# Kernel tuning notes

Measured on AMD Instinct MI355X. Metric: run time of the kernel, lower is better.

The kernel has to match this reference:

```python
import jax, jax.numpy as jnp
import numpy as np

N_HEAD = 16


def setup_inputs() -> dict:
    key = jax.random.key(0)
    k1, k2, k3 = jax.random.split(key, 3)
    B, T, C = 2, 2048, 1024
    x = jax.random.normal(k1, (B, T, C), dtype=jnp.float32)
    Wqkv = jax.random.normal(k2, (C, 3 * C), dtype=jnp.float32) * 0.02
    bqkv = jnp.zeros((3 * C,), dtype=jnp.float32)
    Wproj = jax.random.normal(k3, (C, C), dtype=jnp.float32) * 0.02
    bproj = jnp.zeros((C,), dtype=jnp.float32)
    return {"x": x, "Wqkv": Wqkv, "bqkv": bqkv, "Wproj": Wproj, "bproj": bproj}


def reference(x, Wqkv, bqkv, Wproj, bproj):
    b, t, c = x.shape
    h = N_HEAD
    d = c // h  # head_dim
    # qkv projection, split into q,k,v per head: (b,t,3,h,d)
    qkv = (x @ Wqkv + bqkv).reshape(b, t, 3, h, d)
    q, k, v = qkv[:, :, 0], qkv[:, :, 1], qkv[:, :, 2]  # each (b,t,h,d)
    # Faithful quirk of original: n_state = head_dim // heads, scale = 1/sqrt(n_state)
    scale = jnp.float32(1.0 / np.sqrt(d // h))
    # attn_mode == 'all': dense non-causal attention
    w = jnp.einsum('bqhd,bkhd->bhqk', q, k)  # (b,h,t,t)
    w = jax.nn.softmax(w * scale, axis=-1)
    a = jnp.einsum('bhqk,bkhd->bqhd', w, v).reshape(b, t, c)
    return a @ Wproj + bproj
```

## Files before the change

kernel.cpp:

```cpp
#include <hip/hip_runtime.h>

typedef float floatx4 __attribute__((ext_vector_type(4)));
typedef __bf16 bf16x8 __attribute__((ext_vector_type(8)));
typedef __bf16 bf16x4 __attribute__((ext_vector_type(4)));

#define MFMA16 __builtin_amdgcn_mfma_f32_16x16x32_bf16

typedef const __attribute__((address_space(1))) void* gas_t;
typedef __attribute__((address_space(3))) void* las_t;
#define GLD16(g, l) __builtin_amdgcn_global_load_lds((gas_t)(g), (las_t)(l), 16, 0, 0)

static __device__ __forceinline__ unsigned short f2bf(float f) {
  union { float f; unsigned int u; } v; v.f = f;
  unsigned int r = v.u + 0x7fffu + ((v.u >> 16) & 1u);
  return (unsigned short)(r >> 16);
}

static __device__ __forceinline__ void cast_transpose_tile(
    const float* __restrict__ in, unsigned short* __restrict__ out,
    int R, int C, int bx, int by) {
  const int r0 = by * 64, c0 = bx * 64;
  const int tid = threadIdx.x;
  __shared__ float tl[64][65];
  const int rr = tid >> 4, cc = (tid & 15) * 4;
#pragma unroll
  for (int i = 0; i < 4; ++i) {
    int row = rr + i * 16;
    float4 v = *(const float4*)(in + (size_t)(r0 + row) * C + c0 + cc);
    tl[row][cc] = v.x; tl[row][cc + 1] = v.y;
    tl[row][cc + 2] = v.z; tl[row][cc + 3] = v.w;
  }
  __syncthreads();
  const int cl = tid >> 2, rbase = (tid & 3) * 16;
  unsigned short o[16];
#pragma unroll
  for (int j = 0; j < 16; ++j) o[j] = f2bf(tl[rbase + j][cl]);
  unsigned short* dst = out + (size_t)(c0 + cl) * R + r0 + rbase;
  *(uint4*)dst = *(uint4*)o;
  *(uint4*)(dst + 8) = *(uint4*)(o + 8);
}

__global__ __launch_bounds__(256) void prologue_kernel(
    const float* __restrict__ x, unsigned short* __restrict__ Xb,
    const float* __restrict__ Wqkv, unsigned short* __restrict__ Wqkvt,
    const float* __restrict__ Wproj, unsigned short* __restrict__ Wprojt) {
  const int bid = blockIdx.x;
  if (bid < 4096) {
    int i = bid * 256 + threadIdx.x;
    float4 v = ((const float4*)x)[i];
    ushort4 o;
    o.x = f2bf(v.x); o.y = f2bf(v.y); o.z = f2bf(v.z); o.w = f2bf(v.w);
    ((ushort4*)Xb)[i] = o;
  } else if (bid < 4096 + 768) {
    int b2 = bid - 4096;
    cast_transpose_tile(Wqkv, Wqkvt, 1024, 3072, b2 % 48, b2 / 48);
  } else {
    int b3 = bid - 4096 - 768;
    cast_transpose_tile(Wproj, Wprojt, 1024, 1024, b3 % 16, b3 / 16);
  }
}

__global__ __launch_bounds__(256) void gemm_qkv(
    const unsigned short* __restrict__ A,
    const unsigned short* __restrict__ Bt,
    const float* __restrict__ bias,
    unsigned short* __restrict__ Q,
    unsigned short* __restrict__ Kc,
    unsigned short* __restrict__ Vt) {
  const int K = 1024;
  const int m0 = blockIdx.y * 128, n0 = blockIdx.x * 128;
  const int tid = threadIdx.x, w = tid >> 6, l = tid & 63;
  const int l16 = l & 15, lq = l >> 4;
  const int wm = w >> 1, wn = w & 1;
  const int which = n0 >> 10;

  __shared__ unsigned short As[128 * 64];
  __shared__ unsigned short Bs[128 * 64];

  floatx4 acc[4][4] = {};

  int sA[4], sB[4];
  unsigned ldso[4];
#pragma unroll
  for (int j = 0; j < 4; ++j) {
    int s = j * 256 + tid;
    int row = s >> 3, blk = (s & 7) ^ (row & 7);
    sA[j] = (m0 + row) * K + blk * 8;
    sB[j] = (n0 + row) * K + blk * 8;
    ldso[j] = (unsigned)(j * 256 + w * 64) * 8;
  }

  if (which == 2) {
    for (int k0 = 0; k0 < K; k0 += 64) {
      __syncthreads();
#pragma unroll
      for (int j = 0; j < 4; ++j) {
        GLD16(A + sA[j] + k0, As + ldso[j]);
        GLD16(Bt + sB[j] + k0, Bs + ldso[j]);
      }
      __syncthreads();
#pragma unroll
      for (int kk = 0; kk < 2; ++kk) {
        bf16x8 af[4], bf[4];
#pragma unroll
        for (int mi = 0; mi < 4; ++mi) {
          int row = wm * 64 + mi * 16 + l16;
          int blk = (kk * 4 + lq) ^ (l16 & 7);
          af[mi] = *(const bf16x8*)(As + row * 64 + blk * 8);
        }
#pragma unroll
        for (int ni = 0; ni < 4; ++ni) {
          int row = wn * 64 + ni * 16 + l16;
          int blk = (kk * 4 + lq) ^ (l16 & 7);
          bf[ni] = *(const bf16x8*)(Bs + row * 64 + blk * 8);
        }
#pragma unroll
        for (int ni = 0; ni < 4; ++ni)
#pragma unroll
          for (int mi = 0; mi < 4; ++mi)
            acc[mi][ni] = MFMA16(af[mi], bf[ni], acc[mi][ni], 0, 0, 0);
      }
    }
    float bv[4];
#pragma unroll
    for (int ni = 0; ni < 4; ++ni) bv[ni] = bias[n0 + wn * 64 + ni * 16 + l16];
#pragma unroll
    for (int mi = 0; mi < 4; ++mi) {
#pragma unroll
      for (int ni = 0; ni < 4; ++ni) {
        int col = n0 + wn * 64 + ni * 16 + l16;
        int c1 = col & 1023;
        int h = c1 >> 6, dd = c1 & 63;
        int row0 = m0 + wm * 64 + mi * 16 + lq * 4;
        int bb = row0 >> 11, tt0 = row0 & 2047;
        size_t bh = (size_t)(bb * 16 + h);
        floatx4 vv = acc[mi][ni] + bv[ni];
        *(bf16x4*)(Vt + (bh * 64 + dd) * 2048 + tt0) =
            __builtin_convertvector(vv, bf16x4);
      }
    }
  } else {
    for (int k0 = 0; k0 < K; k0 += 64) {
      __syncthreads();
#pragma unroll
      for (int j = 0; j < 4; ++j) {
        GLD16(A + sA[j] + k0, As + ldso[j]);
        GLD16(Bt + sB[j] + k0, Bs + ldso[j]);
      }
      __syncthreads();
#pragma unroll
      for (int kk = 0; kk < 2; ++kk) {
        bf16x8 af[4], bf[4];
#pragma unroll
        for (int mi = 0; mi < 4; ++mi) {
          int row = wm * 64 + mi * 16 + l16;
          int blk = (kk * 4 + lq) ^ (l16 & 7);
          af[mi] = *(const bf16x8*)(As + row * 64 + blk * 8);
        }
#pragma unroll
        for (int ni = 0; ni < 4; ++ni) {
          int row = wn * 64 + ni * 16 + l16;
          int blk = (kk * 4 + lq) ^ (l16 & 7);
          bf[ni] = *(const bf16x8*)(Bs + row * 64 + blk * 8);
        }
#pragma unroll
        for (int ni = 0; ni < 4; ++ni)
#pragma unroll
          for (int mi = 0; mi < 4; ++mi)
            acc[mi][ni] = MFMA16(bf[ni], af[mi], acc[mi][ni], 0, 0, 0);
      }
    }
    const float sc = (which == 0) ? 0.7213475204444817f : 1.0f;
    unsigned short* dst = (which == 0) ? Q : Kc;
#pragma unroll
    for (int mi = 0; mi < 4; ++mi) {
      int t_g = m0 + wm * 64 + mi * 16 + l16;
      int bb = t_g >> 11, tt = t_g & 2047;
#pragma unroll
      for (int ni = 0; ni < 4; ++ni) {
        int col0 = n0 + wn * 64 + ni * 16 + lq * 4;
        floatx4 bv = *(const floatx4*)(bias + col0);
        floatx4 vv = (acc[mi][ni] + bv) * sc;
        int h = (col0 & 1023) >> 6, dd0 = col0 & 63;
        size_t bh = (size_t)(bb * 16 + h);
        *(bf16x4*)(dst + (bh * 2048 + tt) * 64 + dd0) =
            __builtin_convertvector(vv, bf16x4);
      }
    }
  }
}

__global__ __launch_bounds__(512, 2) void attn_kernel(
    const unsigned short* __restrict__ Q,
    const unsigned short* __restrict__ Kc,
    const unsigned short* __restrict__ Vt,
    unsigned short* __restrict__ AO) {
  const int T = 2048;
  const int bh = blockIdx.y, q0 = blockIdx.x * 256;
  const int tid = threadIdx.x, w = tid >> 6, l = tid & 63;
  const int l16 = l & 15, lq = l >> 4;
  const int kh = w >> 2, wq = w & 3;
  const int h256 = tid & 255;

  __shared__ unsigned short KVs[2][2][2][4096];
  __shared__ unsigned short Ps[8][64 * 64];
  __shared__ float Lx[4][4][64];

  bf16x8 qf[4][2];
  {
    const unsigned short* qb = Q + ((size_t)bh * T + q0 + wq * 64) * 64;
#pragma unroll
    for (int qs = 0; qs < 4; ++qs) {
      const unsigned short* qr = qb + (qs * 16 + l16) * 64;
      qf[qs][0] = *(const bf16x8*)(qr + lq * 8);
      qf[qs][1] = *(const bf16x8*)(qr + 32 + lq * 8);
    }
  }

  float l_lane[4] = {0.f, 0.f, 0.f, 0.f};
  floatx4 o_acc[4][4] = {};

  const unsigned short* kbase = Kc + (size_t)bh * T * 64;
  const unsigned short* vbase = Vt + (size_t)bh * 64 * T;
  int kro[2], vro[2];
  unsigned ldso[2];
#pragma unroll
  for (int j = 0; j < 2; ++j) {
    int s = j * 256 + h256;
    int row = s >> 3, blk = (s & 7) ^ (row & 7);
    kro[j] = row * 64 + blk * 8;
    vro[j] = row * T + blk * 8;
    ldso[j] = (unsigned)(j * 256 + wq * 64) * 8;
  }

  const int swz0 = (0 + lq) ^ (l16 & 7);
  const int swz1 = (4 + lq) ^ (l16 & 7);
  unsigned short* pw = Ps[w];

  {
    int c0 = kh * 16;
#pragma unroll
    for (int j = 0; j < 2; ++j) {
      GLD16(kbase + c0 * 4096 + kro[j], &KVs[0][kh][0][ldso[j]]);
      GLD16(vbase + c0 * 64 + vro[j], &KVs[1][kh][0][ldso[j]]);
    }
  }

  for (int it = 0; it < 16; ++it) {
    __syncthreads();
    if (it + 1 < 16) {
      int cn = kh * 16 + it + 1, nb = (it + 1) & 1;
#pragma unroll
      for (int j = 0; j < 2; ++j) {
        GLD16(kbase + cn * 4096 + kro[j], &KVs[0][kh][nb][ldso[j]]);
        GLD16(vbase + cn * 64 + vro[j], &KVs[1][kh][nb][ldso[j]]);
      }
    }
    const unsigned short* kb = KVs[0][kh][it & 1];
    const unsigned short* vb = KVs[1][kh][it & 1];

    bf16x8 kf[4][2];
#pragma unroll
    for (int ct = 0; ct < 4; ++ct) {
      const unsigned short* kr = kb + (ct * 16 + l16) * 64;
      kf[ct][0] = *(const bf16x8*)(kr + swz0 * 8);
      kf[ct][1] = *(const bf16x8*)(kr + swz1 * 8);
    }

#pragma unroll
    for (int qp = 0; qp < 2; ++qp) {
      floatx4 st[2][4];
#pragma unroll
      for (int ct = 0; ct < 4; ++ct)
#pragma unroll
        for (int q2 = 0; q2 < 2; ++q2) {
          int qs = qp * 2 + q2;
          floatx4 z = {};
          z = MFMA16(kf[ct][0], qf[qs][0], z, 0, 0, 0);
          z = MFMA16(kf[ct][1], qf[qs][1], z, 0, 0, 0);
          st[q2][ct] = z;
        }
#pragma unroll
      for (int q2 = 0; q2 < 2; ++q2) {
        int qs = qp * 2 + q2;
#pragma unroll
        for (int ct = 0; ct < 4; ++ct) {
          floatx4 pv;
          pv[0] = __builtin_amdgcn_exp2f(st[q2][ct][0]);
          pv[1] = __builtin_amdgcn_exp2f(st[q2][ct][1]);
          pv[2] = __builtin_amdgcn_exp2f(st[q2][ct][2]);
          pv[3] = __builtin_amdgcn_exp2f(st[q2][ct][3]);
          l_lane[qs] += (pv[0] + pv[1]) + (pv[2] + pv[3]);
          bf16x4 pb = __builtin_convertvector(pv, bf16x4);
          int blk16 = (ct * 2 + (lq >> 1)) ^ (l16 & 7);
          *(bf16x4*)(pw + (qs * 16 + l16) * 64 + blk16 * 8 + (lq & 1) * 4) =
              pb;
        }
      }
    }

    bf16x8 pf[4][2];
#pragma unroll
    for (int qs = 0; qs < 4; ++qs)
#pragma unroll
      for (int c2 = 0; c2 < 2; ++c2) {
        int blkr = (c2 * 4 + lq) ^ (l16 & 7);
        pf[qs][c2] = *(const bf16x8*)(pw + (qs * 16 + l16) * 64 + blkr * 8);
      }

#pragma unroll
    for (int dt = 0; dt < 4; ++dt) {
      const unsigned short* vr = vb + (dt * 16 + l16) * 64;
      bf16x8 vf0 = *(const bf16x8*)(vr + swz0 * 8);
      bf16x8 vf1 = *(const bf16x8*)(vr + swz1 * 8);
#pragma unroll
      for (int qs = 0; qs < 4; ++qs) {
        o_acc[dt][qs] = MFMA16(vf0, pf[qs][0], o_acc[dt][qs], 0, 0, 0);
        o_acc[dt][qs] = MFMA16(vf1, pf[qs][1], o_acc[dt][qs], 0, 0, 0);
      }
    }
  }

  __syncthreads();
  float* ex = (float*)&KVs[0][0][0][0];
  if (kh == 1) {
    float* r = ex + wq * 4096;
#pragma unroll
    for (int dt = 0; dt < 4; ++dt)
#pragma unroll
      for (int qs = 0; qs < 4; ++qs)
        *(floatx4*)(r + ((dt * 4 + qs) * 64 + l) * 4) = o_acc[dt][qs];
#pragma unroll
    for (int qs = 0; qs < 4; ++qs) Lx[wq][qs][l] = l_lane[qs];
  }
  __syncthreads();
  if (kh == 0) {
    const float* r = ex + wq * 4096;
    const int b = bh >> 4, h = bh & 15;
#pragma unroll
    for (int qs = 0; qs < 4; ++qs) {
      float ls = l_lane[qs] + Lx[wq][qs][l];
      ls += __shfl_xor(ls, 16, 64);
      ls += __shfl_xor(ls, 32, 64);
      float inv = 1.0f / ls;
      int t = q0 + wq * 64 + qs * 16 + l16;
#pragma unroll
      for (int dt = 0; dt < 4; ++dt) {
        floatx4 ov = o_acc[dt][qs] +
                     *(const floatx4*)(r + ((dt * 4 + qs) * 64 + l) * 4);
        ov *= inv;
        bf16x4 ob = __builtin_convertvector(ov, bf16x4);
        *(bf16x4*)(AO + ((size_t)b * 2048 + t) * 1024 + h * 64 + dt * 16 +
                   lq * 4) = ob;
      }
    }
  }
}

__global__ __launch_bounds__(256) void gemm_proj(
    const unsigned short* __restrict__ A,
    const unsigned short* __restrict__ Bt,
    const float* __restrict__ bias,
    float* __restrict__ out) {
  const int K = 1024, N = 1024;
  const int m0 = blockIdx.y * 128, n0 = blockIdx.x * 64;
  const int tid = threadIdx.x, w = tid >> 6, l = tid & 63;
  const int l16 = l & 15, lq = l >> 4;

  __shared__ unsigned short As[128 * 64];
  __shared__ unsigned short Bs[64 * 64];

  floatx4 acc[2][4] = {};

  int sA[4], sB[2];
  unsigned ldsoA[4], ldsoB[2];
#pragma unroll
  for (int j = 0; j < 4; ++j) {
    int s = j * 256 + tid;
    int row = s >> 3, blk = (s & 7) ^ (row & 7);
    sA[j] = (m0 + row) * K + blk * 8;
    ldsoA[j] = (unsigned)(j * 256 + w * 64) * 8;
  }
#pragma unroll
  for (int j = 0; j < 2; ++j) {
    int s = j * 256 + tid;
    int row = s >> 3, blk = (s & 7) ^ (row & 7);
    sB[j] = (n0 + row) * K + blk * 8;
    ldsoB[j] = (unsigned)(j * 256 + w * 64) * 8;
  }

  for (int k0 = 0; k0 < K; k0 += 64) {
    __syncthreads();
#pragma unroll
    for (int j = 0; j < 4; ++j) GLD16(A + sA[j] + k0, As + ldsoA[j]);
#pragma unroll
    for (int j = 0; j < 2; ++j) GLD16(Bt + sB[j] + k0, Bs + ldsoB[j]);
    __syncthreads();
#pragma unroll
    for (int kk = 0; kk < 2; ++kk) {
      bf16x8 af[2], bf[4];
#pragma unroll
      for (int mi = 0; mi < 2; ++mi) {
        int row = w * 32 + mi * 16 + l16;
        int blk = (kk * 4 + lq) ^ (l16 & 7);
        af[mi] = *(const bf16x8*)(As + row * 64 + blk * 8);
      }
#pragma unroll
      for (int ni = 0; ni < 4; ++ni) {
        int row = ni * 16 + l16;
        int blk = (kk * 4 + lq) ^ (l16 & 7);
        bf[ni] = *(const bf16x8*)(Bs + row * 64 + blk * 8);
      }
#pragma unroll
      for (int ni = 0; ni < 4; ++ni)
#pragma unroll
        for (int mi = 0; mi < 2; ++mi)
          acc[mi][ni] = MFMA16(bf[ni], af[mi], acc[mi][ni], 0, 0, 0);
    }
  }

#pragma unroll
  for (int mi = 0; mi < 2; ++mi) {
    int t = m0 + w * 32 + mi * 16 + l16;
#pragma unroll
    for (int ni = 0; ni < 4; ++ni) {
      int col0 = n0 + ni * 16 + lq * 4;
      floatx4 bv = *(const floatx4*)(bias + col0);
      *(floatx4*)(out + (size_t)t * N + col0) = acc[mi][ni] + bv;
    }
  }
}

extern "C" void kernel_launch(void* const* d_in, const int* in_sizes, int n_in,
                              void* d_out, int out_size, void* d_ws,
                              size_t ws_size, hipStream_t stream) {
  const float* x     = (const float*)d_in[0];
  const float* Wqkv  = (const float*)d_in[1];
  const float* bqkv  = (const float*)d_in[2];
  const float* Wproj = (const float*)d_in[3];
  const float* bproj = (const float*)d_in[4];
  float* out = (float*)d_out;

  unsigned short* Xb     = (unsigned short*)d_ws;
  unsigned short* Wqkvt  = Xb + 4194304;
  unsigned short* Wprojt = Wqkvt + 3145728;
  unsigned short* Qb     = Wprojt + 1048576;
  unsigned short* Kb     = Qb + 4194304;
  unsigned short* Vtb    = Kb + 4194304;
  unsigned short* AOb    = Vtb + 4194304;

  prologue_kernel<<<5120, 256, 0, stream>>>(x, Xb, Wqkv, Wqkvt, Wproj, Wprojt);
  gemm_qkv<<<dim3(24, 32), 256, 0, stream>>>(Xb, Wqkvt, bqkv, Qb, Kb, Vtb);
  attn_kernel<<<dim3(8, 32), 512, 0, stream>>>(Qb, Kb, Vtb, AOb);
  gemm_proj<<<dim3(16, 32), 256, 0, stream>>>(AOb, Wprojt, bproj, out);
}
```

Baseline: 195.7 us.

## Stage QKV epilogue through LDS for coalesced stores and halve attention block size

The QKV GEMM epilogue now writes each wave's tile into an LDS scratch area and then emits 16-byte coalesced global stores for Q, K and the transposed V, instead of scattered 8-byte stores. The attention kernel drops from 512 to 256 threads per block with 128 queries per block, doubling the grid to 512 blocks to fill more CUs. It also shrinks the P scratch buffer to one 16-row slice per wave, computing and consuming P per query subtile. The staging adds an extra barrier and LDS round trip, and smaller attention blocks reload K/V tiles twice as often.

```diff
diff --git a/kernel.cpp b/kernel.cpp
--- a/kernel.cpp
+++ b/kernel.cpp
@@ -74,8 +74,9 @@
   const int wm = w >> 1, wn = w & 1;
   const int which = n0 >> 10;
 
-  __shared__ unsigned short As[128 * 64];
-  __shared__ unsigned short Bs[128 * 64];
+  __shared__ __align__(16) unsigned short SH[16384];
+  unsigned short* As = SH;
+  unsigned short* Bs = SH + 8192;
 
   floatx4 acc[4][4] = {};
 
@@ -124,19 +125,28 @@
     float bv[4];
 #pragma unroll
     for (int ni = 0; ni < 4; ++ni) bv[ni] = bias[n0 + wn * 64 + ni * 16 + l16];
-#pragma unroll
-    for (int mi = 0; mi < 4; ++mi) {
-#pragma unroll
-      for (int ni = 0; ni < 4; ++ni) {
-        int col = n0 + wn * 64 + ni * 16 + l16;
-        int c1 = col & 1023;
-        int h = c1 >> 6, dd = c1 & 63;
-        int row0 = m0 + wm * 64 + mi * 16 + lq * 4;
-        int bb = row0 >> 11, tt0 = row0 & 2047;
-        size_t bh = (size_t)(bb * 16 + h);
-        floatx4 vv = acc[mi][ni] + bv[ni];
-        *(bf16x4*)(Vt + (bh * 64 + dd) * 2048 + tt0) =
-            __builtin_convertvector(vv, bf16x4);
+    __syncthreads();
+    unsigned short* E = SH + w * 2304;
+    const int bh = (m0 >> 11) * 16 + ((n0 & 1023) >> 6) + wn;
+    const int tt0 = (m0 & 2047) + wm * 64;
+#pragma unroll
+    for (int p = 0; p < 2; ++p) {
+#pragma unroll
+      for (int n2 = 0; n2 < 2; ++n2) {
+        int ni = p * 2 + n2;
+#pragma unroll
+        for (int mi = 0; mi < 4; ++mi) {
+          floatx4 vv = acc[mi][ni] + bv[ni];
+          *(bf16x4*)(E + (n2 * 16 + l16) * 72 + mi * 16 + lq * 4) =
+              __builtin_convertvector(vv, bf16x4);
+        }
+      }
+#pragma unroll
+      for (int s = 0; s < 4; ++s) {
+        int dl = s * 8 + (l >> 3);
+        bf16x8 vv = *(const bf16x8*)(E + dl * 72 + (l & 7) * 8);
+        *(bf16x8*)(Vt + ((size_t)bh * 64 + p * 32 + dl) * 2048 + tt0 +
+                   (l & 7) * 8) = vv;
       }
     }
   } else {
@@ -172,39 +182,49 @@
     }
     const float sc = (which == 0) ? 0.7213475204444817f : 1.0f;
     unsigned short* dst = (which == 0) ? Q : Kc;
-#pragma unroll
-    for (int mi = 0; mi < 4; ++mi) {
-      int t_g = m0 + wm * 64 + mi * 16 + l16;
-      int bb = t_g >> 11, tt = t_g & 2047;
-#pragma unroll
-      for (int ni = 0; ni < 4; ++ni) {
-        int col0 = n0 + wn * 64 + ni * 16 + lq * 4;
-        floatx4 bv = *(const floatx4*)(bias + col0);
-        floatx4 vv = (acc[mi][ni] + bv) * sc;
-        int h = (col0 & 1023) >> 6, dd0 = col0 & 63;
-        size_t bh = (size_t)(bb * 16 + h);
-        *(bf16x4*)(dst + (bh * 2048 + tt) * 64 + dd0) =
-            __builtin_convertvector(vv, bf16x4);
-      }
-    }
-  }
-}
-
-__global__ __launch_bounds__(512, 2) void attn_kernel(
+    __syncthreads();
+    unsigned short* E = SH + w * 2304;
+    const int bh = (m0 >> 11) * 16 + ((n0 & 1023) >> 6) + wn;
+    const size_t gbase = ((size_t)bh * 2048 + (m0 & 2047) + wm * 64) * 64;
+#pragma unroll
+    for (int p = 0; p < 2; ++p) {
+#pragma unroll
+      for (int m2 = 0; m2 < 2; ++m2) {
+        int mi = p * 2 + m2;
+#pragma unroll
+        for (int ni = 0; ni < 4; ++ni) {
+          int col0 = n0 + wn * 64 + ni * 16 + lq * 4;
+          floatx4 bv = *(const floatx4*)(bias + col0);
+          floatx4 vv = (acc[mi][ni] + bv) * sc;
+          *(bf16x4*)(E + (m2 * 16 + l16) * 72 + ni * 16 + lq * 4) =
+              __builtin_convertvector(vv, bf16x4);
+        }
+      }
+#pragma unroll
+      for (int s = 0; s < 4; ++s) {
+        int rl = s * 8 + (l >> 3);
+        bf16x8 vv = *(const bf16x8*)(E + rl * 72 + (l & 7) * 8);
+        *(bf16x8*)(dst + gbase + (size_t)(p * 32 + rl) * 64 + (l & 7) * 8) =
+            vv;
+      }
+    }
+  }
+}
+
+__global__ __launch_bounds__(256, 2) void attn_kernel(
     const unsigned short* __restrict__ Q,
     const unsigned short* __restrict__ Kc,
     const unsigned short* __restrict__ Vt,
     unsigned short* __restrict__ AO) {
   const int T = 2048;
-  const int bh = blockIdx.y, q0 = blockIdx.x * 256;
+  const int bh = blockIdx.y, q0 = blockIdx.x * 128;
   const int tid = threadIdx.x, w = tid >> 6, l = tid & 63;
   const int l16 = l & 15, lq = l >> 4;
-  const int kh = w >> 2, wq = w & 3;
-  const int h256 = tid & 255;
-
-  __shared__ unsigned short KVs[2][2][2][4096];
-  __shared__ unsigned short Ps[8][64 * 64];
-  __shared__ float Lx[4][4][64];
+  const int kh = w >> 1, wq = w & 1;
+  const int h128 = tid & 127;
+
+  __shared__ __align__(16) unsigned short KVs[2][2][2][4096];
+  __shared__ __align__(16) unsigned short Ps[4][1024];
 
   bf16x8 qf[4][2];
   {
@@ -222,15 +242,15 @@
 
   const unsigned short* kbase = Kc + (size_t)bh * T * 64;
   const unsigned short* vbase = Vt + (size_t)bh * 64 * T;
-  int kro[2], vro[2];
-  unsigned ldso[2];
-#pragma unroll
-  for (int j = 0; j < 2; ++j) {
-    int s = j * 256 + h256;
+  int kro[4], vro[4];
+  unsigned ldso[4];
+#pragma unroll
+  for (int j = 0; j < 4; ++j) {
+    int s = j * 128 + h128;
     int row = s >> 3, blk = (s & 7) ^ (row & 7);
     kro[j] = row * 64 + blk * 8;
     vro[j] = row * T + blk * 8;
-    ldso[j] = (unsigned)(j * 256 + wq * 64) * 8;
+    ldso[j] = (unsigned)(j * 128 + wq * 64) * 8;
   }
 
   const int swz0 = (0 + lq) ^ (l16 & 7);
@@ -240,7 +260,7 @@
   {
     int c0 = kh * 16;
 #pragma unroll
-    for (int j = 0; j < 2; ++j) {
+    for (int j = 0; j < 4; ++j) {
       GLD16(kbase + c0 * 4096 + kro[j], &KVs[0][kh][0][ldso[j]]);
       GLD16(vbase + c0 * 64 + vro[j], &KVs[1][kh][0][ldso[j]]);
     }
@@ -251,7 +271,7 @@
     if (it + 1 < 16) {
       int cn = kh * 16 + it + 1, nb = (it + 1) & 1;
 #pragma unroll
-      for (int j = 0; j < 2; ++j) {
+      for (int j = 0; j < 4; ++j) {
         GLD16(kbase + cn * 4096 + kro[j], &KVs[0][kh][nb][ldso[j]]);
         GLD16(vbase + cn * 64 + vro[j], &KVs[1][kh][nb][ldso[j]]);
       }
@@ -267,46 +287,35 @@
       kf[ct][1] = *(const bf16x8*)(kr + swz1 * 8);
     }
 
-#pragma unroll
-    for (int qp = 0; qp < 2; ++qp) {
-      floatx4 st[2][4];
-#pragma unroll
-      for (int ct = 0; ct < 4; ++ct)
-#pragma unroll
-        for (int q2 = 0; q2 < 2; ++q2) {
-          int qs = qp * 2 + q2;
-          floatx4 z = {};
-          z = MFMA16(kf[ct][0], qf[qs][0], z, 0, 0, 0);
-          z = MFMA16(kf[ct][1], qf[qs][1], z, 0, 0, 0);
-          st[q2][ct] = z;
-        }
-#pragma unroll
-      for (int q2 = 0; q2 < 2; ++q2) {
-        int qs = qp * 2 + q2;
-#pragma unroll
-        for (int ct = 0; ct < 4; ++ct) {
-          floatx4 pv;
-          pv[0] = __builtin_amdgcn_exp2f(st[q2][ct][0]);
-          pv[1] = __builtin_amdgcn_exp2f(st[q2][ct][1]);
-          pv[2] = __builtin_amdgcn_exp2f(st[q2][ct][2]);
-          pv[3] = __builtin_amdgcn_exp2f(st[q2][ct][3]);
-          l_lane[qs] += (pv[0] + pv[1]) + (pv[2] + pv[3]);
-          bf16x4 pb = __builtin_convertvector(pv, bf16x4);
-          int blk16 = (ct * 2 + (lq >> 1)) ^ (l16 & 7);
-          *(bf16x4*)(pw + (qs * 16 + l16) * 64 + blk16 * 8 + (lq & 1) * 4) =
-              pb;
-        }
-      }
-    }
-
     bf16x8 pf[4][2];
 #pragma unroll
-    for (int qs = 0; qs < 4; ++qs)
+    for (int qs = 0; qs < 4; ++qs) {
+      floatx4 st[4];
+#pragma unroll
+      for (int ct = 0; ct < 4; ++ct) {
+        floatx4 z = {};
+        z = MFMA16(kf[ct][0], qf[qs][0], z, 0, 0, 0);
+        z = MFMA16(kf[ct][1], qf[qs][1], z, 0, 0, 0);
+        st[ct] = z;
+      }
+#pragma unroll
+      for (int ct = 0; ct < 4; ++ct) {
+        floatx4 pv;
+        pv[0] = __builtin_amdgcn_exp2f(st[ct][0]);
+        pv[1] = __builtin_amdgcn_exp2f(st[ct][1]);
+        pv[2] = __builtin_amdgcn_exp2f(st[ct][2]);
+        pv[3] = __builtin_amdgcn_exp2f(st[ct][3]);
+        l_lane[qs] += (pv[0] + pv[1]) + (pv[2] + pv[3]);
+        bf16x4 pb = __builtin_convertvector(pv, bf16x4);
+        int blk16 = (ct * 2 + (lq >> 1)) ^ (l16 & 7);
+        *(bf16x4*)(pw + l16 * 64 + blk16 * 8 + (lq & 1) * 4) = pb;
+      }
 #pragma unroll
       for (int c2 = 0; c2 < 2; ++c2) {
         int blkr = (c2 * 4 + lq) ^ (l16 & 7);
-        pf[qs][c2] = *(const bf16x8*)(pw + (qs * 16 + l16) * 64 + blkr * 8);
-      }
+        pf[qs][c2] = *(const bf16x8*)(pw + l16 * 64 + blkr * 8);
+      }
+    }
 
 #pragma unroll
     for (int dt = 0; dt < 4; ++dt) {
@@ -323,6 +332,7 @@
 
   __syncthreads();
   float* ex = (float*)&KVs[0][0][0][0];
+  float* Lx = (float*)&Ps[0][0];
   if (kh == 1) {
     float* r = ex + wq * 4096;
 #pragma unroll
@@ -331,7 +341,7 @@
       for (int qs = 0; qs < 4; ++qs)
         *(floatx4*)(r + ((dt * 4 + qs) * 64 + l) * 4) = o_acc[dt][qs];
 #pragma unroll
-    for (int qs = 0; qs < 4; ++qs) Lx[wq][qs][l] = l_lane[qs];
+    for (int qs = 0; qs < 4; ++qs) Lx[(wq * 4 + qs) * 64 + l] = l_lane[qs];
   }
   __syncthreads();
   if (kh == 0) {
@@ -339,7 +349,7 @@
     const int b = bh >> 4, h = bh & 15;
 #pragma unroll
     for (int qs = 0; qs < 4; ++qs) {
-      float ls = l_lane[qs] + Lx[wq][qs][l];
+      float ls = l_lane[qs] + Lx[(wq * 4 + qs) * 64 + l];
       ls += __shfl_xor(ls, 16, 64);
       ls += __shfl_xor(ls, 32, 64);
       float inv = 1.0f / ls;
@@ -367,8 +377,8 @@
   const int tid = threadIdx.x, w = tid >> 6, l = tid & 63;
   const int l16 = l & 15, lq = l >> 4;
 
-  __shared__ unsigned short As[128 * 64];
-  __shared__ unsigned short Bs[64 * 64];
+  __shared__ __align__(16) unsigned short As[128 * 64];
+  __shared__ __align__(16) unsigned short Bs[64 * 64];
 
   floatx4 acc[2][4] = {};
 
@@ -451,6 +461,6 @@
 
   prologue_kernel<<<5120, 256, 0, stream>>>(x, Xb, Wqkv, Wqkvt, Wproj, Wprojt);
   gemm_qkv<<<dim3(24, 32), 256, 0, stream>>>(Xb, Wqkvt, bqkv, Qb, Kb, Vtb);
-  attn_kernel<<<dim3(8, 32), 512, 0, stream>>>(Qb, Kb, Vtb, AOb);
+  attn_kernel<<<dim3(16, 32), 256, 0, stream>>>(Qb, Kb, Vtb, AOb);
   gemm_proj<<<dim3(16, 32), 256, 0, stream>>>(AOb, Wprojt, bproj, out);
 }
```

Measured after the change: 190.4 us. -2.7%, faster.
